# Kernel optimization log

Hardware: AMD Instinct MI355X
Metric: run time of the kernel (lower is better)

Reference implementation:

```python
import jax, jax.numpy as jnp
import numpy as np

NUM_GROUPS = 5
EPS = 1e-5
QB = 128.0  # 2**(8-1) for b=8 activation quantization


def _binarize_weights_groupwise(W):
    """Sign-binarize W group-wise along out-feature dim, STE on backward.
    Faithful to torch: rows beyond num_groups*group_size remain zero."""
    n_out = W.shape[0]
    gs = n_out // NUM_GROUPS
    Wb = jnp.zeros_like(W)
    for g in range(NUM_GROUPS):  # small fixed loop (5 groups)
        wg = W[g * gs:(g + 1) * gs]
        z = wg - wg.mean()
        # STE: forward = sign(z), backward = identity w.r.t. z
        ste = z + jax.lax.stop_gradient(jnp.sign(z) - z)
        Wb = Wb.at[g * gs:(g + 1) * gs].set(ste)
    return Wb


def _quantize_activations_groupwise(x):
    """8-bit absmax quantization group-wise along dim 0 (batch), per torch code."""
    n = x.shape[0]
    gs = n // NUM_GROUPS
    xq = jnp.zeros_like(x)
    for g in range(NUM_GROUPS):
        ag = x[g * gs:(g + 1) * gs]
        gamma = jnp.max(jnp.abs(ag))
        xq = xq.at[g * gs:(g + 1) * gs].set(
            jnp.clip(ag * QB / (gamma + EPS), -QB + EPS, QB - EPS))
    return xq


def _bitlinear(x, W, b):
    Wb = _binarize_weights_groupwise(W)
    y = jnp.einsum('btc,oc->bto', x, Wb) + b
    return _quantize_activations_groupwise(y)


def setup_inputs() -> dict:
    key = jax.random.key(0)
    k1, k2, k3, k4, k5 = jax.random.split(key, 5)
    B, T, C = 10, 2048, 384
    H = 4 * C
    lim1 = 1.0 / np.sqrt(C)
    lim2 = 1.0 / np.sqrt(H)
    x = jax.random.normal(k1, (B, T, C), dtype=jnp.float32)
    W1 = jax.random.uniform(k2, (H, C), minval=-lim1, maxval=lim1, dtype=jnp.float32)
    b1 = jax.random.uniform(k3, (H,), minval=-lim1, maxval=lim1, dtype=jnp.float32)
    W2 = jax.random.uniform(k4, (C, H), minval=-lim2, maxval=lim2, dtype=jnp.float32)
    b2 = jax.random.uniform(k5, (C,), minval=-lim2, maxval=lim2, dtype=jnp.float32)
    return {"x": x, "W1": W1, "b1": b1, "W2": W2, "b2": b2}


def reference(x, W1, b1, W2, b2):
    h = _bitlinear(x, W1, b1)           # [B,T,4C], quantized to [-128,128]
    h = jax.nn.gelu(h, approximate=False)  # torch nn.GELU default is exact
    out = _bitlinear(h, W2, b2)         # [B,T,C]
    return out  # nn.Dropout is identity in eval/reference mode
```

## Files before the change

### kernel.cpp

```cpp
#include <hip/hip_runtime.h>
#include <cstdint>
#include <cstddef>

#define THREADS 256
#define NB 8

typedef float f32x4 __attribute__((ext_vector_type(4)));
typedef __bf16 bf16x8 __attribute__((ext_vector_type(8)));
typedef __bf16 bf16x4 __attribute__((ext_vector_type(4)));

__device__ __forceinline__ void gload_lds16(const void* g, void* l) {
    auto gp = (const __attribute__((address_space(1))) unsigned int*)(unsigned long long)(uintptr_t)g;
    auto lp = (__attribute__((address_space(3))) unsigned int*)(unsigned int)(uintptr_t)l;
    __builtin_amdgcn_global_load_lds(gp, lp, 16, 0, 0);
}

__global__ void zero_gamma(unsigned int* p) {
    if (threadIdx.x < 16) p[threadIdx.x] = 0u;
}

__global__ void group_partial_sums(const float* __restrict__ W, float* __restrict__ partials,
                                   int elems_per_group) {
    const int g = blockIdx.y, b = blockIdx.x;
    const int tid = threadIdx.x;
    const int chunk4 = elems_per_group / (4 * NB);
    const float* base = W + (size_t)g * elems_per_group + (size_t)b * chunk4 * 4;
    float s = 0.f;
    for (int i = tid; i < chunk4; i += THREADS) {
        f32x4 v = *reinterpret_cast<const f32x4*>(base + 4 * (size_t)i);
        s += (v[0] + v[1]) + (v[2] + v[3]);
    }
    __shared__ float red[THREADS];
    red[tid] = s;
    __syncthreads();
    for (int off = THREADS / 2; off > 0; off >>= 1) {
        if (tid < off) red[tid] += red[tid + off];
        __syncthreads();
    }
    if (tid == 0) partials[g * NB + b] = red[0];
}

__global__ void binarize_apply(const float* __restrict__ W, __bf16* __restrict__ Wb,
                               const float* __restrict__ partials,
                               int elems_per_group, int tail_elems) {
    const int g = blockIdx.y, b = blockIdx.x;
    const int tid = threadIdx.x;
    if (g == 5) {
        if (b != 0) return;
        __bf16* og = Wb + (size_t)5 * elems_per_group;
        for (int i = tid; i < tail_elems; i += THREADS) og[i] = (__bf16)0.f;
        return;
    }
    float total = 0.f;
#pragma unroll
    for (int j = 0; j < NB; ++j) total += partials[g * NB + j];
    const float mean = total / (float)elems_per_group;

    const int chunk4 = elems_per_group / (4 * NB);
    const size_t off0 = (size_t)g * elems_per_group + (size_t)b * chunk4 * 4;
    const float* base = W + off0;
    __bf16* ob = Wb + off0;
    for (int i = tid; i < chunk4; i += THREADS) {
        f32x4 v = *reinterpret_cast<const f32x4*>(base + 4 * (size_t)i);
        bf16x4 o;
#pragma unroll
        for (int j = 0; j < 4; ++j) {
            const float z = v[j] - mean;
            o[j] = (__bf16)((z > 0.f) ? 1.f : ((z < 0.f) ? -1.f : 0.f));
        }
        *reinterpret_cast<bf16x4*>(ob + 4 * (size_t)i) = o;
    }
}

__global__ void cvt_f32_bf16(const float* __restrict__ in, __bf16* __restrict__ ot, int n4) {
    int i = blockIdx.x * blockDim.x + threadIdx.x;
    if (i >= n4) return;
    f32x4 v = *reinterpret_cast<const f32x4*>(in + 4 * (size_t)i);
    bf16x4 o;
    o[0] = (__bf16)v[0]; o[1] = (__bf16)v[1]; o[2] = (__bf16)v[2]; o[3] = (__bf16)v[3];
    *reinterpret_cast<bf16x4*>(ot + 4 * (size_t)i) = o;
}

template<int BN_, int OUT_BF16>
__global__ __launch_bounds__(512, 2)
void gemm_bt2(const __bf16* __restrict__ A, const __bf16* __restrict__ Bw,
              const float* __restrict__ bias, void* __restrict__ outp,
              unsigned int* __restrict__ gmax, int M, int N, int K,
              int GN, int nwg) {
    constexpr int BM = 256, BK = 64;
    constexpr int NF = BN_ / 64;
    constexpr int ABYTES = BM * BK * 2;
    constexpr int BBYTES = BN_ * BK * 2;
    constexpr int AR = ABYTES / (512 * 16);
    constexpr int BR = BBYTES / (512 * 16);
    __shared__ __attribute__((aligned(16))) char lds[2 * (ABYTES + BBYTES)];

    const int tid = threadIdx.x;
    const int wave = tid >> 6, lane = tid & 63;
    const int l15 = lane & 15, l4 = lane >> 4;
    const int wr = wave >> 2, wc = wave & 3;

    const int cpx = nwg >> 3;
    const int orig = (blockIdx.x & 7) * cpx + (blockIdx.x >> 3);
    const int bm = orig / GN, bn = orig % GN;

    const __bf16* Ab = A + (size_t)bm * BM * K;
    const __bf16* Bb = Bw + (size_t)bn * BN_ * K;
    const int NT = K / BK;

    f32x4 acc[8][NF];
#pragma unroll
    for (int m = 0; m < 8; ++m)
#pragma unroll
        for (int n = 0; n < NF; ++n)
            acc[m][n] = f32x4{0.f, 0.f, 0.f, 0.f};

    auto STAGE = [&](int t, int b) {
        const int k0 = t * BK;
        char* ab = lds + b * (ABYTES + BBYTES);
        char* bb = ab + ABYTES;
#pragma unroll
        for (int j = 0; j < AR; ++j) {
            const int q = j * 8192 + tid * 16;
            const int row = q >> 7;
            const int slot = (q >> 4) & 7;
            gload_lds16(Ab + (size_t)row * K + k0 + ((slot ^ (row & 7)) << 3), ab + q);
        }
#pragma unroll
        for (int j = 0; j < BR; ++j) {
            const int q = j * 8192 + tid * 16;
            const int row = q >> 7;
            const int slot = (q >> 4) & 7;
            gload_lds16(Bb + (size_t)row * K + k0 + ((slot ^ (row & 7)) << 3), bb + q);
        }
    };

    STAGE(0, 0);
    asm volatile("s_waitcnt vmcnt(0)" ::: "memory");
    __syncthreads();

    for (int t = 0; t < NT; ++t) {
        const int b = t & 1;
        if (t + 1 < NT) STAGE(t + 1, b ^ 1);
        const char* ab = lds + b * (ABYTES + BBYTES);
        const char* bb = ab + ABYTES;
#pragma unroll
        for (int kk = 0; kk < BK; kk += 32) {
            const int s0 = (kk >> 3) + l4;
            bf16x8 af[8], bfv[NF];
#pragma unroll
            for (int m = 0; m < 8; ++m) {
                const int r = wr * 128 + m * 16 + l15;
                af[m] = *reinterpret_cast<const bf16x8*>(
                    ab + r * 128 + ((s0 ^ (r & 7)) << 4));
            }
#pragma unroll
            for (int n = 0; n < NF; ++n) {
                const int r = wc * (BN_ / 4) + n * 16 + l15;
                bfv[n] = *reinterpret_cast<const bf16x8*>(
                    bb + r * 128 + ((s0 ^ (r & 7)) << 4));
            }
#pragma unroll
            for (int m = 0; m < 8; ++m)
#pragma unroll
                for (int n = 0; n < NF; ++n)
                    acc[m][n] = __builtin_amdgcn_mfma_f32_16x16x32_bf16(
                        af[m], bfv[n], acc[m][n], 0, 0, 0);
        }
        asm volatile("s_waitcnt vmcnt(0)" ::: "memory");
        __syncthreads();
    }

    const int row0 = bm * BM + wr * 128 + l4 * 4;
    const int col0 = bn * BN_ + wc * (BN_ / 4) + l15;
    float lmax = 0.f;
#pragma unroll
    for (int n = 0; n < NF; ++n) {
        const int col = col0 + n * 16;
        const float bv = bias[col];
#pragma unroll
        for (int m = 0; m < 8; ++m) {
#pragma unroll
            for (int r = 0; r < 4; ++r) {
                const int row = row0 + m * 16 + r;
                const float v = acc[m][n][r] + bv;
                lmax = fmaxf(lmax, fabsf(v));
                if (OUT_BF16) ((__bf16*)outp)[(size_t)row * N + col] = (__bf16)v;
                else          ((float*)outp)[(size_t)row * N + col] = v;
            }
        }
    }
#pragma unroll
    for (int off = 32; off > 0; off >>= 1)
        lmax = fmaxf(lmax, __shfl_down(lmax, off, 64));
    float* wredmax = (float*)lds;
    if (lane == 0) wredmax[wave] = lmax;
    __syncthreads();
    if (tid == 0) {
        float bmax = wredmax[0];
#pragma unroll
        for (int w = 1; w < 8; ++w) bmax = fmaxf(bmax, wredmax[w]);
        atomicMax(gmax + (bm * BM) / 4096, __float_as_uint(bmax));
    }
}

__global__ void quant_gelu(__bf16* __restrict__ y, const unsigned int* __restrict__ gbits,
                           int perg8, int n8) {
    int i = blockIdx.x * blockDim.x + threadIdx.x;
    if (i >= n8) return;
    const int g = i / perg8;
    const float gamma = __uint_as_float(gbits[g]);
    const float s = 128.0f / (gamma + 1e-5f);
    bf16x8 v = *reinterpret_cast<const bf16x8*>(y + 8 * (size_t)i);
    bf16x8 o;
#pragma unroll
    for (int j = 0; j < 8; ++j) {
        float f = (float)v[j] * s;
        f = fminf(fmaxf(f, -128.0f + 1e-5f), 128.0f - 1e-5f);
        const float ge = 0.5f * f * (1.0f + erff(f * 0.70710678118654752f));
        o[j] = (__bf16)ge;
    }
    *reinterpret_cast<bf16x8*>(y + 8 * (size_t)i) = o;
}

__global__ void final_scale(float* __restrict__ y, const unsigned int* __restrict__ gbits,
                            int perg4, int n4) {
    int i = blockIdx.x * blockDim.x + threadIdx.x;
    if (i >= n4) return;
    const int g = i / perg4;
    const float gamma = __uint_as_float(gbits[g]);
    const float s = 128.0f / (gamma + 1e-5f);
    f32x4 v = *reinterpret_cast<const f32x4*>(y + 4 * (size_t)i);
    f32x4 o;
#pragma unroll
    for (int j = 0; j < 4; ++j)
        o[j] = fminf(fmaxf(v[j] * s, -128.0f + 1e-5f), 128.0f - 1e-5f);
    *reinterpret_cast<f32x4*>(y + 4 * (size_t)i) = o;
}

extern "C" void kernel_launch(void* const* d_in, const int* in_sizes, int n_in,
                              void* d_out, int out_size, void* d_ws, size_t ws_size,
                              hipStream_t stream) {
    const float* x  = (const float*)d_in[0];
    const float* W1 = (const float*)d_in[1];
    const float* b1 = (const float*)d_in[2];
    const float* W2 = (const float*)d_in[3];
    const float* b2 = (const float*)d_in[4];
    float* out = (float*)d_out;

    const int BB = 10, TT = 2048, C = 384, H = 1536;
    const int M = BB * TT;

    const int gs1 = H / 5;
    const int gs2 = C / 5;
    const int epg1 = gs1 * C;
    const int epg2 = gs2 * H;
    const int tail1 = (H - 5 * gs1) * C;
    const int tail2 = (C - 5 * gs2) * H;

    const size_t szW1b = (size_t)H * C * 2;
    const size_t szW2b = (size_t)C * H * 2;
    const size_t szXb  = (size_t)M * C * 2;
    const size_t szY1  = (size_t)M * H * 2;

    char* p = (char*)d_ws;
    __bf16* W1b = (__bf16*)p; p += szW1b;
    __bf16* W2b = (__bf16*)p; p += szW2b;
    __bf16* xb  = (__bf16*)p; p += szXb;
    __bf16* y1  = (__bf16*)p; p += szY1;
    unsigned int* gamma = (unsigned int*)p; p += 64;
    float* psums = (float*)p; p += 2 * 5 * NB * 4;
    if ((size_t)(p - (char*)d_ws) > ws_size) return;

    zero_gamma<<<1, 64, 0, stream>>>(gamma);

    group_partial_sums<<<dim3(NB, 5), THREADS, 0, stream>>>(W1, psums, epg1);
    group_partial_sums<<<dim3(NB, 5), THREADS, 0, stream>>>(W2, psums + 5 * NB, epg2);
    binarize_apply<<<dim3(NB, 6), THREADS, 0, stream>>>(W1, W1b, psums, epg1, tail1);
    binarize_apply<<<dim3(NB, 6), THREADS, 0, stream>>>(W2, W2b, psums + 5 * NB, epg2, tail2);

    cvt_f32_bf16<<<(M * C / 4 + THREADS - 1) / THREADS, THREADS, 0, stream>>>(x, xb, M * C / 4);

    gemm_bt2<256, 1><<<480, 512, 0, stream>>>(
        xb, W1b, b1, (void*)y1, gamma, M, H, C, H / 256, 480);

    quant_gelu<<<(M * H / 8 + THREADS - 1) / THREADS, THREADS, 0, stream>>>(
        y1, gamma, (M / 5) * H / 8, M * H / 8);

    gemm_bt2<128, 0><<<240, 512, 0, stream>>>(
        y1, W2b, b2, (void*)out, gamma + 5, M, C, H, C / 128, 240);

    final_scale<<<(M * C / 4 + THREADS - 1) / THREADS, THREADS, 0, stream>>>(
        out, gamma + 5, (M / 5) * C / 4, M * C / 4);
}
```

Baseline: 153.5 us.

## Restructure GEMM main loop into multi-phase pipeline with half-tile staged prefetch

Replaces the simple double-buffered GEMM loop with a four-phase-per-tile schedule. Global-to-LDS loads are split into A and B halves and prefetched up to two tiles ahead, interleaved between MFMA phases. Partial vmcnt waits, per-phase barriers and s_setprio raise MFMA priority. The aim is to hide memory latency and LDS reads behind matrix math, at the cost of more barriers and more complex, fragile address swizzling and LDS layout.

```diff
diff --git a/kernel.cpp b/kernel.cpp
--- a/kernel.cpp
+++ b/kernel.cpp
@@ -83,17 +83,18 @@
 
 template<int BN_, int OUT_BF16>
 __global__ __launch_bounds__(512, 2)
-void gemm_bt2(const __bf16* __restrict__ A, const __bf16* __restrict__ Bw,
+void gemm_8ph(const __bf16* __restrict__ A, const __bf16* __restrict__ Bw,
               const float* __restrict__ bias, void* __restrict__ outp,
               unsigned int* __restrict__ gmax, int M, int N, int K,
               int GN, int nwg) {
     constexpr int BM = 256, BK = 64;
     constexpr int NF = BN_ / 64;
-    constexpr int ABYTES = BM * BK * 2;
-    constexpr int BBYTES = BN_ * BK * 2;
-    constexpr int AR = ABYTES / (512 * 16);
-    constexpr int BR = BBYTES / (512 * 16);
-    __shared__ __attribute__((aligned(16))) char lds[2 * (ABYTES + BBYTES)];
+    constexpr int AHB = 16384;
+    constexpr int BHB = BN_ * 64;
+    constexpr int TILEB = 2 * AHB + 2 * BHB;
+    constexpr int AHR = 2;
+    constexpr int BHR = BHB / 8192;
+    __shared__ __attribute__((aligned(16))) char lds[2 * TILEB];
 
     const int tid = threadIdx.x;
     const int wave = tid >> 6, lane = tid & 63;
@@ -115,60 +116,88 @@
         for (int n = 0; n < NF; ++n)
             acc[m][n] = f32x4{0.f, 0.f, 0.f, 0.f};
 
-    auto STAGE = [&](int t, int b) {
+    auto STAGE_A = [&](int t, int h) {
         const int k0 = t * BK;
-        char* ab = lds + b * (ABYTES + BBYTES);
-        char* bb = ab + ABYTES;
-#pragma unroll
-        for (int j = 0; j < AR; ++j) {
+        char* base = lds + (t & 1) * TILEB + 2 * BHB + h * AHB;
+#pragma unroll
+        for (int j = 0; j < AHR; ++j) {
             const int q = j * 8192 + tid * 16;
-            const int row = q >> 7;
-            const int slot = (q >> 4) & 7;
-            gload_lds16(Ab + (size_t)row * K + k0 + ((slot ^ (row & 7)) << 3), ab + q);
-        }
-#pragma unroll
-        for (int j = 0; j < BR; ++j) {
+            const int lr = q >> 7;
+            const int s = ((q >> 4) & 7) ^ (lr & 7);
+            const int gr = h * 64 + (lr & 63) + ((lr >> 6) << 7);
+            gload_lds16(Ab + (size_t)gr * K + k0 + s * 8, base + q);
+        }
+    };
+    auto STAGE_B = [&](int t, int h) {
+        const int k0 = t * BK;
+        char* base = lds + (t & 1) * TILEB + h * BHB;
+#pragma unroll
+        for (int j = 0; j < BHR; ++j) {
             const int q = j * 8192 + tid * 16;
-            const int row = q >> 7;
-            const int slot = (q >> 4) & 7;
-            gload_lds16(Bb + (size_t)row * K + k0 + ((slot ^ (row & 7)) << 3), bb + q);
+            const int lr = q >> 6;
+            const int s = ((q >> 4) & 3) ^ ((lr >> 1) & 3);
+            gload_lds16(Bb + (size_t)lr * K + k0 + h * 32 + s * 8, base + q);
         }
     };
 
-    STAGE(0, 0);
-    asm volatile("s_waitcnt vmcnt(0)" ::: "memory");
-    __syncthreads();
-
+    STAGE_B(0, 0); STAGE_B(0, 1); STAGE_A(0, 0); STAGE_A(0, 1);
+    if (NT > 1) { STAGE_B(1, 0); STAGE_B(1, 1); STAGE_A(1, 0); }
+    if constexpr (BHR == 2) asm volatile("s_waitcnt vmcnt(6)" ::: "memory");
+    else                    asm volatile("s_waitcnt vmcnt(4)" ::: "memory");
+    __builtin_amdgcn_s_barrier();
+    __builtin_amdgcn_sched_barrier(0);
+
+    bf16x8 bfr[2][NF];
     for (int t = 0; t < NT; ++t) {
-        const int b = t & 1;
-        if (t + 1 < NT) STAGE(t + 1, b ^ 1);
-        const char* ab = lds + b * (ABYTES + BBYTES);
-        const char* bb = ab + ABYTES;
-#pragma unroll
-        for (int kk = 0; kk < BK; kk += 32) {
-            const int s0 = (kk >> 3) + l4;
-            bf16x8 af[8], bfv[NF];
-#pragma unroll
-            for (int m = 0; m < 8; ++m) {
-                const int r = wr * 128 + m * 16 + l15;
-                af[m] = *reinterpret_cast<const bf16x8*>(
-                    ab + r * 128 + ((s0 ^ (r & 7)) << 4));
+        const char* buf = lds + (t & 1) * TILEB;
+#pragma unroll
+        for (int p = 0; p < 4; ++p) {
+            const int kk = p & 1, mb = (p >> 1) * 4;
+            bf16x8 af[4];
+#pragma unroll
+            for (int i = 0; i < 4; ++i) {
+                const int m = mb + i;
+                const int lr = wr * 64 + (m & 3) * 16 + l15;
+                const int sp = (kk * 4 + l4) ^ (lr & 7);
+                af[i] = *reinterpret_cast<const bf16x8*>(
+                    buf + 2 * BHB + (m >> 2) * AHB + lr * 128 + sp * 16);
             }
-#pragma unroll
-            for (int n = 0; n < NF; ++n) {
-                const int r = wc * (BN_ / 4) + n * 16 + l15;
-                bfv[n] = *reinterpret_cast<const bf16x8*>(
-                    bb + r * 128 + ((s0 ^ (r & 7)) << 4));
+            if (p < 2) {
+#pragma unroll
+                for (int n = 0; n < NF; ++n) {
+                    const int lr = wc * (BN_ / 4) + n * 16 + l15;
+                    const int sp = l4 ^ ((lr >> 1) & 3);
+                    bfr[kk][n] = *reinterpret_cast<const bf16x8*>(
+                        buf + kk * BHB + lr * 64 + sp * 16);
+                }
             }
-#pragma unroll
-            for (int m = 0; m < 8; ++m)
+            if (p == 0)      { if (t + 1 < NT) STAGE_A(t + 1, 1); }
+            else if (p == 1) { if (t + 2 < NT) STAGE_B(t + 2, 0); }
+            else if (p == 2) { if (t + 2 < NT) STAGE_B(t + 2, 1); }
+            else             { if (t + 2 < NT) STAGE_A(t + 2, 0); }
+            asm volatile("" ::: "memory");
+            __builtin_amdgcn_s_barrier();
+            __builtin_amdgcn_sched_barrier(0);
+            __builtin_amdgcn_s_setprio(1);
+#pragma unroll
+            for (int i = 0; i < 4; ++i)
 #pragma unroll
                 for (int n = 0; n < NF; ++n)
-                    acc[m][n] = __builtin_amdgcn_mfma_f32_16x16x32_bf16(
-                        af[m], bfv[n], acc[m][n], 0, 0, 0);
-        }
-        asm volatile("s_waitcnt vmcnt(0)" ::: "memory");
-        __syncthreads();
+                    acc[mb + i][n] = __builtin_amdgcn_mfma_f32_16x16x32_bf16(
+                        af[i], bfr[kk][n], acc[mb + i][n], 0, 0, 0);
+            __builtin_amdgcn_s_setprio(0);
+            if (p == 3) {
+                if (t + 2 < NT) {
+                    if constexpr (BHR == 2) asm volatile("s_waitcnt vmcnt(6)" ::: "memory");
+                    else                    asm volatile("s_waitcnt vmcnt(4)" ::: "memory");
+                } else {
+                    asm volatile("s_waitcnt vmcnt(0)" ::: "memory");
+                }
+            }
+            asm volatile("" ::: "memory");
+            __builtin_amdgcn_s_barrier();
+            __builtin_amdgcn_sched_barrier(0);
+        }
     }
 
     const int row0 = bm * BM + wr * 128 + l4 * 4;
@@ -281,13 +310,13 @@
 
     cvt_f32_bf16<<<(M * C / 4 + THREADS - 1) / THREADS, THREADS, 0, stream>>>(x, xb, M * C / 4);
 
-    gemm_bt2<256, 1><<<480, 512, 0, stream>>>(
+    gemm_8ph<256, 1><<<480, 512, 0, stream>>>(
         xb, W1b, b1, (void*)y1, gamma, M, H, C, H / 256, 480);
 
     quant_gelu<<<(M * H / 8 + THREADS - 1) / THREADS, THREADS, 0, stream>>>(
         y1, gamma, (M / 5) * H / 8, M * H / 8);
 
-    gemm_bt2<128, 0><<<240, 512, 0, stream>>>(
+    gemm_8ph<128, 0><<<240, 512, 0, stream>>>(
         y1, W2b, b2, (void*)out, gamma + 5, M, C, H, C / 128, 240);
 
     final_scale<<<(M * C / 4 + THREADS - 1) / THREADS, THREADS, 0, stream>>>(
```

After: 156.6 us, median of 4. Within noise of the previous version (+2.0%).

## Fuse fp32-to-bf16 activation conversion into first GEMM and vectorize epilogue stores

Applied to the files above, without the earlier changes.

Removes the separate cvt_f32_bf16 kernel and its bf16 copy of x. The first GEMM now loads fp32 A tiles into registers, converts them and writes them to swizzled LDS, with B still loaded directly via global_load_lds. Both GEMMs swap the MFMA operand order, so each lane holds four consecutive columns and the epilogue can issue vector stores (bf16x4 / f32x4) with vector bias loads instead of scalar strided stores. In exchange, A now goes through registers, which raises register pressure and makes the first GEMM's prefetch synchronous with the LDS write.

```diff
diff --git a/kernel.cpp b/kernel.cpp
--- a/kernel.cpp
+++ b/kernel.cpp
@@ -72,27 +72,14 @@
     }
 }
 
-__global__ void cvt_f32_bf16(const float* __restrict__ in, __bf16* __restrict__ ot, int n4) {
-    int i = blockIdx.x * blockDim.x + threadIdx.x;
-    if (i >= n4) return;
-    f32x4 v = *reinterpret_cast<const f32x4*>(in + 4 * (size_t)i);
-    bf16x4 o;
-    o[0] = (__bf16)v[0]; o[1] = (__bf16)v[1]; o[2] = (__bf16)v[2]; o[3] = (__bf16)v[3];
-    *reinterpret_cast<bf16x4*>(ot + 4 * (size_t)i) = o;
-}
-
-template<int BN_, int OUT_BF16>
 __global__ __launch_bounds__(512, 2)
-void gemm_bt2(const __bf16* __restrict__ A, const __bf16* __restrict__ Bw,
-              const float* __restrict__ bias, void* __restrict__ outp,
-              unsigned int* __restrict__ gmax, int M, int N, int K,
-              int GN, int nwg) {
-    constexpr int BM = 256, BK = 64;
-    constexpr int NF = BN_ / 64;
+void gemm1_f32a(const float* __restrict__ A, const __bf16* __restrict__ Bw,
+                const float* __restrict__ bias, __bf16* __restrict__ outp,
+                unsigned int* __restrict__ gmax, int M, int N, int K,
+                int GN, int nwg) {
+    constexpr int BM = 256, BN = 256, BK = 64, NF = 4;
     constexpr int ABYTES = BM * BK * 2;
-    constexpr int BBYTES = BN_ * BK * 2;
-    constexpr int AR = ABYTES / (512 * 16);
-    constexpr int BR = BBYTES / (512 * 16);
+    constexpr int BBYTES = BN * BK * 2;
     __shared__ __attribute__((aligned(16))) char lds[2 * (ABYTES + BBYTES)];
 
     const int tid = threadIdx.x;
@@ -104,6 +91,143 @@
     const int orig = (blockIdx.x & 7) * cpx + (blockIdx.x >> 3);
     const int bm = orig / GN, bn = orig % GN;
 
+    const int arow = tid >> 1;
+    const int ach = tid & 1;
+    const float* Aptr = A + (size_t)(bm * BM + arow) * K + ach * 32;
+    const __bf16* Bb = Bw + (size_t)bn * BN * K;
+    const int NT = K / BK;
+
+    f32x4 acc[8][NF];
+#pragma unroll
+    for (int m = 0; m < 8; ++m)
+#pragma unroll
+        for (int n = 0; n < NF; ++n)
+            acc[m][n] = f32x4{0.f, 0.f, 0.f, 0.f};
+
+    f32x4 areg[8];
+    auto LOADA = [&](int t) {
+        const float* p = Aptr + t * BK;
+#pragma unroll
+        for (int j = 0; j < 8; ++j)
+            areg[j] = *reinterpret_cast<const f32x4*>(p + j * 4);
+    };
+    auto WRITEA = [&](int t) {
+        char* ab = lds + (t & 1) * (ABYTES + BBYTES);
+#pragma unroll
+        for (int j = 0; j < 4; ++j) {
+            bf16x8 w;
+#pragma unroll
+            for (int e = 0; e < 4; ++e) {
+                w[e]     = (__bf16)areg[2 * j][e];
+                w[e + 4] = (__bf16)areg[2 * j + 1][e];
+            }
+            const int s = ach * 4 + j;
+            *reinterpret_cast<bf16x8*>(
+                ab + arow * 128 + ((s ^ (arow & 7)) << 4)) = w;
+        }
+    };
+    auto STAGEB = [&](int t) {
+        char* bb = lds + (t & 1) * (ABYTES + BBYTES) + ABYTES;
+#pragma unroll
+        for (int j = 0; j < 4; ++j) {
+            const int q = j * 8192 + tid * 16;
+            const int lr = q >> 7;
+            const int s = ((q >> 4) & 7) ^ (lr & 7);
+            gload_lds16(Bb + (size_t)lr * K + t * BK + s * 8, bb + q);
+        }
+    };
+
+    LOADA(0); STAGEB(0);
+    asm volatile("s_waitcnt vmcnt(0)" ::: "memory");
+    WRITEA(0);
+    __syncthreads();
+
+    for (int t = 0; t < NT; ++t) {
+        if (t + 1 < NT) { LOADA(t + 1); STAGEB(t + 1); }
+        const char* ab = lds + (t & 1) * (ABYTES + BBYTES);
+        const char* bb = ab + ABYTES;
+#pragma unroll
+        for (int kk = 0; kk < 2; ++kk) {
+            bf16x8 af[8], bfv[NF];
+#pragma unroll
+            for (int m = 0; m < 8; ++m) {
+                const int r = wr * 128 + m * 16 + l15;
+                const int sp = (kk * 4 + l4) ^ (r & 7);
+                af[m] = *reinterpret_cast<const bf16x8*>(ab + r * 128 + sp * 16);
+            }
+#pragma unroll
+            for (int n = 0; n < NF; ++n) {
+                const int r = wc * 64 + n * 16 + l15;
+                const int sp = (kk * 4 + l4) ^ (r & 7);
+                bfv[n] = *reinterpret_cast<const bf16x8*>(bb + r * 128 + sp * 16);
+            }
+#pragma unroll
+            for (int m = 0; m < 8; ++m)
+#pragma unroll
+                for (int n = 0; n < NF; ++n)
+                    acc[m][n] = __builtin_amdgcn_mfma_f32_16x16x32_bf16(
+                        bfv[n], af[m], acc[m][n], 0, 0, 0);
+        }
+        if (t + 1 < NT) {
+            asm volatile("s_waitcnt vmcnt(0)" ::: "memory");
+            WRITEA(t + 1);
+        }
+        __syncthreads();
+    }
+
+    const int rowb = bm * BM + wr * 128;
+    const int colb = bn * BN + wc * 64;
+    float lmax = 0.f;
+#pragma unroll
+    for (int n = 0; n < NF; ++n) {
+        const f32x4 bv = *reinterpret_cast<const f32x4*>(bias + colb + n * 16 + l4 * 4);
+#pragma unroll
+        for (int m = 0; m < 8; ++m) {
+            const int row = rowb + m * 16 + l15;
+            bf16x4 o;
+#pragma unroll
+            for (int r = 0; r < 4; ++r) {
+                const float v = acc[m][n][r] + bv[r];
+                lmax = fmaxf(lmax, fabsf(v));
+                o[r] = (__bf16)v;
+            }
+            *reinterpret_cast<bf16x4*>(
+                &outp[(size_t)row * N + colb + n * 16 + l4 * 4]) = o;
+        }
+    }
+#pragma unroll
+    for (int off = 32; off > 0; off >>= 1)
+        lmax = fmaxf(lmax, __shfl_down(lmax, off, 64));
+    float* wredmax = (float*)lds;
+    if (lane == 0) wredmax[wave] = lmax;
+    __syncthreads();
+    if (tid == 0) {
+        float bmax = wredmax[0];
+#pragma unroll
+        for (int w = 1; w < 8; ++w) bmax = fmaxf(bmax, wredmax[w]);
+        atomicMax(gmax + (bm * BM) / 4096, __float_as_uint(bmax));
+    }
+}
+
+__global__ __launch_bounds__(512, 2)
+void gemm2_bt(const __bf16* __restrict__ A, const __bf16* __restrict__ Bw,
+              const float* __restrict__ bias, float* __restrict__ outp,
+              unsigned int* __restrict__ gmax, int M, int N, int K,
+              int GN, int nwg) {
+    constexpr int BM = 256, BN_ = 128, BK = 64, NF = 2;
+    constexpr int ABYTES = BM * BK * 2;
+    constexpr int BBYTES = BN_ * BK * 2;
+    __shared__ __attribute__((aligned(16))) char lds[2 * (ABYTES + BBYTES)];
+
+    const int tid = threadIdx.x;
+    const int wave = tid >> 6, lane = tid & 63;
+    const int l15 = lane & 15, l4 = lane >> 4;
+    const int wr = wave >> 2, wc = wave & 3;
+
+    const int cpx = nwg >> 3;
+    const int orig = (blockIdx.x & 7) * cpx + (blockIdx.x >> 3);
+    const int bm = orig / GN, bn = orig % GN;
+
     const __bf16* Ab = A + (size_t)bm * BM * K;
     const __bf16* Bb = Bw + (size_t)bn * BN_ * K;
     const int NT = K / BK;
@@ -115,79 +239,77 @@
         for (int n = 0; n < NF; ++n)
             acc[m][n] = f32x4{0.f, 0.f, 0.f, 0.f};
 
-    auto STAGE = [&](int t, int b) {
+    auto STAGE = [&](int t) {
         const int k0 = t * BK;
-        char* ab = lds + b * (ABYTES + BBYTES);
+        char* ab = lds + (t & 1) * (ABYTES + BBYTES);
         char* bb = ab + ABYTES;
 #pragma unroll
-        for (int j = 0; j < AR; ++j) {
+        for (int j = 0; j < 4; ++j) {
             const int q = j * 8192 + tid * 16;
-            const int row = q >> 7;
-            const int slot = (q >> 4) & 7;
-            gload_lds16(Ab + (size_t)row * K + k0 + ((slot ^ (row & 7)) << 3), ab + q);
-        }
-#pragma unroll
-        for (int j = 0; j < BR; ++j) {
+            const int lr = q >> 7;
+            const int s = ((q >> 4) & 7) ^ (lr & 7);
+            gload_lds16(Ab + (size_t)lr * K + k0 + s * 8, ab + q);
+        }
+#pragma unroll
+        for (int j = 0; j < 2; ++j) {
             const int q = j * 8192 + tid * 16;
-            const int row = q >> 7;
-            const int slot = (q >> 4) & 7;
-            gload_lds16(Bb + (size_t)row * K + k0 + ((slot ^ (row & 7)) << 3), bb + q);
+            const int lr = q >> 7;
+            const int s = ((q >> 4) & 7) ^ (lr & 7);
+            gload_lds16(Bb + (size_t)lr * K + k0 + s * 8, bb + q);
         }
     };
 
-    STAGE(0, 0);
+    STAGE(0);
     asm volatile("s_waitcnt vmcnt(0)" ::: "memory");
     __syncthreads();
 
     for (int t = 0; t < NT; ++t) {
-        const int b = t & 1;
-        if (t + 1 < NT) STAGE(t + 1, b ^ 1);
-        const char* ab = lds + b * (ABYTES + BBYTES);
+        if (t + 1 < NT) STAGE(t + 1);
+        const char* ab = lds + (t & 1) * (ABYTES + BBYTES);
         const char* bb = ab + ABYTES;
 #pragma unroll
-        for (int kk = 0; kk < BK; kk += 32) {
-            const int s0 = (kk >> 3) + l4;
+        for (int kk = 0; kk < 2; ++kk) {
             bf16x8 af[8], bfv[NF];
 #pragma unroll
             for (int m = 0; m < 8; ++m) {
                 const int r = wr * 128 + m * 16 + l15;
-                af[m] = *reinterpret_cast<const bf16x8*>(
-                    ab + r * 128 + ((s0 ^ (r & 7)) << 4));
+                const int sp = (kk * 4 + l4) ^ (r & 7);
+                af[m] = *reinterpret_cast<const bf16x8*>(ab + r * 128 + sp * 16);
             }
 #pragma unroll
             for (int n = 0; n < NF; ++n) {
-                const int r = wc * (BN_ / 4) + n * 16 + l15;
-                bfv[n] = *reinterpret_cast<const bf16x8*>(
-                    bb + r * 128 + ((s0 ^ (r & 7)) << 4));
+                const int r = wc * 32 + n * 16 + l15;
+                const int sp = (kk * 4 + l4) ^ (r & 7);
+                bfv[n] = *reinterpret_cast<const bf16x8*>(bb + r * 128 + sp * 16);
             }
 #pragma unroll
             for (int m = 0; m < 8; ++m)
 #pragma unroll
                 for (int n = 0; n < NF; ++n)
                     acc[m][n] = __builtin_amdgcn_mfma_f32_16x16x32_bf16(
-                        af[m], bfv[n], acc[m][n], 0, 0, 0);
+                        bfv[n], af[m], acc[m][n], 0, 0, 0);
         }
         asm volatile("s_waitcnt vmcnt(0)" ::: "memory");
         __syncthreads();
     }
 
-    const int row0 = bm * BM + wr * 128 + l4 * 4;
-    const int col0 = bn * BN_ + wc * (BN_ / 4) + l15;
+    const int rowb = bm * BM + wr * 128;
+    const int colb = bn * BN_ + wc * 32;
     float lmax = 0.f;
 #pragma unroll
     for (int n = 0; n < NF; ++n) {
-        const int col = col0 + n * 16;
-        const float bv = bias[col];
+        const f32x4 bv = *reinterpret_cast<const f32x4*>(bias + colb + n * 16 + l4 * 4);
 #pragma unroll
         for (int m = 0; m < 8; ++m) {
+            const int row = rowb + m * 16 + l15;
+            f32x4 o;
 #pragma unroll
             for (int r = 0; r < 4; ++r) {
-                const int row = row0 + m * 16 + r;
-                const float v = acc[m][n][r] + bv;
-                lmax = fmaxf(lmax, fabsf(v));
-                if (OUT_BF16) ((__bf16*)outp)[(size_t)row * N + col] = (__bf16)v;
-                else          ((float*)outp)[(size_t)row * N + col] = v;
-            }
+                o[r] = acc[m][n][r] + bv[r];
+                lmax = fmaxf(lmax, fabsf(o[r]));
+            }
+            *reinterpret_cast<f32x4*>(
+                &outp[(size_t)row * N + colb + n * 16 + l4 * 4]) = o;
         }
     }
 #pragma unroll
@@ -260,13 +382,11 @@
 
     const size_t szW1b = (size_t)H * C * 2;
     const size_t szW2b = (size_t)C * H * 2;
-    const size_t szXb  = (size_t)M * C * 2;
     const size_t szY1  = (size_t)M * H * 2;
 
     char* p = (char*)d_ws;
     __bf16* W1b = (__bf16*)p; p += szW1b;
     __bf16* W2b = (__bf16*)p; p += szW2b;
-    __bf16* xb  = (__bf16*)p; p += szXb;
     __bf16* y1  = (__bf16*)p; p += szY1;
     unsigned int* gamma = (unsigned int*)p; p += 64;
     float* psums = (float*)p; p += 2 * 5 * NB * 4;
@@ -279,16 +399,14 @@
     binarize_apply<<<dim3(NB, 6), THREADS, 0, stream>>>(W1, W1b, psums, epg1, tail1);
     binarize_apply<<<dim3(NB, 6), THREADS, 0, stream>>>(W2, W2b, psums + 5 * NB, epg2, tail2);
 
-    cvt_f32_bf16<<<(M * C / 4 + THREADS - 1) / THREADS, THREADS, 0, stream>>>(x, xb, M * C / 4);
-
-    gemm_bt2<256, 1><<<480, 512, 0, stream>>>(
-        xb, W1b, b1, (void*)y1, gamma, M, H, C, H / 256, 480);
+    gemm1_f32a<<<480, 512, 0, stream>>>(
+        x, W1b, b1, y1, gamma, M, H, C, H / 256, 480);
 
     quant_gelu<<<(M * H / 8 + THREADS - 1) / THREADS, THREADS, 0, stream>>>(
         y1, gamma, (M / 5) * H / 8, M * H / 8);
 
-    gemm_bt2<128, 0><<<240, 512, 0, stream>>>(
-        y1, W2b, b2, (void*)out, gamma + 5, M, C, H, C / 128, 240);
+    gemm2_bt<<<240, 512, 0, stream>>>(
+        y1, W2b, b2, out, gamma + 5, M, C, H, C / 128, 240);
 
     final_scale<<<(M * C / 4 + THREADS - 1) / THREADS, THREADS, 0, stream>>>(
         out, gamma + 5, (M / 5) * C / 4, M * C / 4);
```

After: 162.9 us. 6.1% more time.

## Fuse final quantization into second GEMM via cooperative grid sync; vectorize epilogue stores

Applied to the files above, without the earlier changes.

The second GEMM now runs as a cooperative kernel. It keeps its accumulators in registers, synchronizes the whole grid after the per-group absmax atomics, then applies the scale and clamp and writes the final output once. This removes the separate final_scale pass, which read and rewrote the fp32 output. The MFMA operands are swapped so each lane holds four consecutive columns, which lets the epilogue issue vectorized 16-byte and 8-byte stores instead of scalar ones. The cost is a grid-wide barrier and the requirement that all 240 blocks be co-resident.

```diff
diff --git a/kernel.cpp b/kernel.cpp
--- a/kernel.cpp
+++ b/kernel.cpp
@@ -1,6 +1,9 @@
 #include <hip/hip_runtime.h>
+#include <hip/hip_cooperative_groups.h>
 #include <cstdint>
 #include <cstddef>
+
+namespace cg = cooperative_groups;
 
 #define THREADS 256
 #define NB 8
@@ -81,9 +84,9 @@
     *reinterpret_cast<bf16x4*>(ot + 4 * (size_t)i) = o;
 }
 
-template<int BN_, int OUT_BF16>
+template<int BN_, int OUT_BF16, int COOP>
 __global__ __launch_bounds__(512, 2)
-void gemm_bt2(const __bf16* __restrict__ A, const __bf16* __restrict__ Bw,
+void gemm_bt3(const __bf16* __restrict__ A, const __bf16* __restrict__ Bw,
               const float* __restrict__ bias, void* __restrict__ outp,
               unsigned int* __restrict__ gmax, int M, int N, int K,
               int GN, int nwg) {
@@ -115,78 +118,85 @@
         for (int n = 0; n < NF; ++n)
             acc[m][n] = f32x4{0.f, 0.f, 0.f, 0.f};
 
-    auto STAGE = [&](int t, int b) {
+    auto STAGE = [&](int t) {
         const int k0 = t * BK;
-        char* ab = lds + b * (ABYTES + BBYTES);
+        char* ab = lds + (t & 1) * (ABYTES + BBYTES);
         char* bb = ab + ABYTES;
 #pragma unroll
         for (int j = 0; j < AR; ++j) {
             const int q = j * 8192 + tid * 16;
-            const int row = q >> 7;
-            const int slot = (q >> 4) & 7;
-            gload_lds16(Ab + (size_t)row * K + k0 + ((slot ^ (row & 7)) << 3), ab + q);
+            const int lr = q >> 7;
+            const int s = ((q >> 4) & 7) ^ (lr & 7);
+            gload_lds16(Ab + (size_t)lr * K + k0 + s * 8, ab + q);
         }
 #pragma unroll
         for (int j = 0; j < BR; ++j) {
             const int q = j * 8192 + tid * 16;
-            const int row = q >> 7;
-            const int slot = (q >> 4) & 7;
-            gload_lds16(Bb + (size_t)row * K + k0 + ((slot ^ (row & 7)) << 3), bb + q);
+            const int lr = q >> 7;
+            const int s = ((q >> 4) & 7) ^ (lr & 7);
+            gload_lds16(Bb + (size_t)lr * K + k0 + s * 8, bb + q);
         }
     };
 
-    STAGE(0, 0);
+    STAGE(0);
     asm volatile("s_waitcnt vmcnt(0)" ::: "memory");
     __syncthreads();
 
     for (int t = 0; t < NT; ++t) {
-        const int b = t & 1;
-        if (t + 1 < NT) STAGE(t + 1, b ^ 1);
-        const char* ab = lds + b * (ABYTES + BBYTES);
+        if (t + 1 < NT) STAGE(t + 1);
+        const char* ab = lds + (t & 1) * (ABYTES + BBYTES);
         const char* bb = ab + ABYTES;
 #pragma unroll
-        for (int kk = 0; kk < BK; kk += 32) {
-            const int s0 = (kk >> 3) + l4;
+        for (int kk = 0; kk < 2; ++kk) {
             bf16x8 af[8], bfv[NF];
 #pragma unroll
             for (int m = 0; m < 8; ++m) {
                 const int r = wr * 128 + m * 16 + l15;
-                af[m] = *reinterpret_cast<const bf16x8*>(
-                    ab + r * 128 + ((s0 ^ (r & 7)) << 4));
+                const int sp = (kk * 4 + l4) ^ (r & 7);
+                af[m] = *reinterpret_cast<const bf16x8*>(ab + r * 128 + sp * 16);
             }
 #pragma unroll
             for (int n = 0; n < NF; ++n) {
                 const int r = wc * (BN_ / 4) + n * 16 + l15;
-                bfv[n] = *reinterpret_cast<const bf16x8*>(
-                    bb + r * 128 + ((s0 ^ (r & 7)) << 4));
+                const int sp = (kk * 4 + l4) ^ (r & 7);
+                bfv[n] = *reinterpret_cast<const bf16x8*>(bb + r * 128 + sp * 16);
             }
 #pragma unroll
             for (int m = 0; m < 8; ++m)
 #pragma unroll
                 for (int n = 0; n < NF; ++n)
                     acc[m][n] = __builtin_amdgcn_mfma_f32_16x16x32_bf16(
-                        af[m], bfv[n], acc[m][n], 0, 0, 0);
+                        bfv[n], af[m], acc[m][n], 0, 0, 0);
         }
         asm volatile("s_waitcnt vmcnt(0)" ::: "memory");
         __syncthreads();
     }
 
-    const int row0 = bm * BM + wr * 128 + l4 * 4;
-    const int col0 = bn * BN_ + wc * (BN_ / 4) + l15;
+    const int rowb = bm * BM + wr * 128;
+    const int colb = bn * BN_ + wc * (BN_ / 4);
     float lmax = 0.f;
 #pragma unroll
     for (int n = 0; n < NF; ++n) {
-        const int col = col0 + n * 16;
-        const float bv = bias[col];
+        const f32x4 bv = *reinterpret_cast<const f32x4*>(bias + colb + n * 16 + l4 * 4);
 #pragma unroll
         for (int m = 0; m < 8; ++m) {
 #pragma unroll
             for (int r = 0; r < 4; ++r) {
-                const int row = row0 + m * 16 + r;
-                const float v = acc[m][n][r] + bv;
-                lmax = fmaxf(lmax, fabsf(v));
-                if (OUT_BF16) ((__bf16*)outp)[(size_t)row * N + col] = (__bf16)v;
-                else          ((float*)outp)[(size_t)row * N + col] = v;
+                acc[m][n][r] += bv[r];
+                lmax = fmaxf(lmax, fabsf(acc[m][n][r]));
+            }
+            if constexpr (!COOP) {
+                const int row = rowb + m * 16 + l15;
+                if (OUT_BF16) {
+                    bf16x4 o;
+#pragma unroll
+                    for (int r = 0; r < 4; ++r) o[r] = (__bf16)acc[m][n][r];
+                    *reinterpret_cast<bf16x4*>(
+                        &((__bf16*)outp)[(size_t)row * N + colb + n * 16 + l4 * 4]) = o;
+                } else {
+                    *reinterpret_cast<f32x4*>(
+                        &((float*)outp)[(size_t)row * N + colb + n * 16 + l4 * 4]) = acc[m][n];
+                }
             }
         }
     }
@@ -201,6 +211,27 @@
 #pragma unroll
         for (int w = 1; w < 8; ++w) bmax = fmaxf(bmax, wredmax[w]);
         atomicMax(gmax + (bm * BM) / 4096, __float_as_uint(bmax));
+    }
+
+    if constexpr (COOP) {
+        cg::this_grid().sync();
+        const float g = __uint_as_float(
+            *(volatile unsigned int*)(gmax + (bm * BM) / 4096));
+        const float s = 128.0f / (g + 1e-5f);
+#pragma unroll
+        for (int n = 0; n < NF; ++n) {
+#pragma unroll
+            for (int m = 0; m < 8; ++m) {
+                const int row = rowb + m * 16 + l15;
+                f32x4 o;
+#pragma unroll
+                for (int r = 0; r < 4; ++r)
+                    o[r] = fminf(fmaxf(acc[m][n][r] * s, -128.0f + 1e-5f),
+                                 128.0f - 1e-5f);
+                *reinterpret_cast<f32x4*>(
+                    &((float*)outp)[(size_t)row * N + colb + n * 16 + l4 * 4]) = o;
+            }
+        }
     }
 }
 
@@ -223,21 +254,6 @@
     *reinterpret_cast<bf16x8*>(y + 8 * (size_t)i) = o;
 }
 
-__global__ void final_scale(float* __restrict__ y, const unsigned int* __restrict__ gbits,
-                            int perg4, int n4) {
-    int i = blockIdx.x * blockDim.x + threadIdx.x;
-    if (i >= n4) return;
-    const int g = i / perg4;
-    const float gamma = __uint_as_float(gbits[g]);
-    const float s = 128.0f / (gamma + 1e-5f);
-    f32x4 v = *reinterpret_cast<const f32x4*>(y + 4 * (size_t)i);
-    f32x4 o;
-#pragma unroll
-    for (int j = 0; j < 4; ++j)
-        o[j] = fminf(fmaxf(v[j] * s, -128.0f + 1e-5f), 128.0f - 1e-5f);
-    *reinterpret_cast<f32x4*>(y + 4 * (size_t)i) = o;
-}
-
 extern "C" void kernel_launch(void* const* d_in, const int* in_sizes, int n_in,
                               void* d_out, int out_size, void* d_ws, size_t ws_size,
                               hipStream_t stream) {
@@ -281,15 +297,21 @@
 
     cvt_f32_bf16<<<(M * C / 4 + THREADS - 1) / THREADS, THREADS, 0, stream>>>(x, xb, M * C / 4);
 
-    gemm_bt2<256, 1><<<480, 512, 0, stream>>>(
+    gemm_bt3<256, 1, 0><<<480, 512, 0, stream>>>(
         xb, W1b, b1, (void*)y1, gamma, M, H, C, H / 256, 480);
 
     quant_gelu<<<(M * H / 8 + THREADS - 1) / THREADS, THREADS, 0, stream>>>(
         y1, gamma, (M / 5) * H / 8, M * H / 8);
 
-    gemm_bt2<128, 0><<<240, 512, 0, stream>>>(
-        y1, W2b, b2, (void*)out, gamma + 5, M, C, H, C / 128, 240);
-
-    final_scale<<<(M * C / 4 + THREADS - 1) / THREADS, THREADS, 0, stream>>>(
-        out, gamma + 5, (M / 5) * C / 4, M * C / 4);
-}
+    {
+        const __bf16* a_ = y1;
+        const __bf16* w_ = W2b;
+        const float* bias_ = b2;
+        void* out_ = (void*)out;
+        unsigned int* gm_ = gamma + 5;
+        int M_ = M, N_ = C, K_ = H, GN_ = C / 128, nwg_ = 240;
+        void* args[] = {&a_, &w_, &bias_, &out_, &gm_, &M_, &N_, &K_, &GN_, &nwg_};
+        hipLaunchCooperativeKernel((void*)gemm_bt3<128, 0, 1>,
+                                   dim3(240), dim3(512), args, 0, stream);
+    }
+}
```

Result: slower. 179.4 us (+16.8%).
